# Kernel optimization log

Hardware: AMD Instinct MI355X
Metric: run time of the kernel (lower is better)

The kernel has to match this reference:

```python
import jax, jax.numpy as jnp
import numpy as np
import math

N = 131072        # number of query points
IN_DIM = 3
G = 5             # grid_level = num_sin_layers - 2
F = 8             # feature_dims per level
W = 256           # hidden width (ffenc_dims[1:])
OUT = 64          # num_outputs
BOUND = 1.0
BASE_SIGMA = 1.0
EXP_SIGMA = 2.0
SIN_W0 = 5.0      # multires - 1 = n_levels - 1


def setup_inputs() -> dict:
    key = jax.random.key(0)
    ks = jax.random.split(key, 9)
    in_pos = jax.random.uniform(ks[0], (N, IN_DIM), jnp.float32, -BOUND, BOUND)
    grid_feats = jax.random.normal(ks[1], (N, G * F), jnp.float32) * 0.01  # grid_embed_std
    ffn_A = jax.random.normal(ks[2], (G, F, W), jnp.float32)
    # SIREN-style inits (scaled normals approximating uniform SIREN init ranges)
    W0 = jax.random.normal(ks[3], (IN_DIM, W), jnp.float32) / IN_DIM
    b0 = jax.random.normal(ks[4], (W,), jnp.float32) * 0.01
    Wh = jax.random.normal(ks[5], (G, W, W), jnp.float32) * (math.sqrt(6.0 / W) / SIN_W0)
    bh = jax.random.normal(ks[6], (G, W), jnp.float32) * 0.01
    Wh_high = jax.random.normal(ks[7], (G, W, OUT), jnp.float32) * (math.sqrt(6.0 / W) / SIN_W0)
    bh_high = jax.random.normal(ks[8], (G, OUT), jnp.float32) * 0.01
    return {"in_pos": in_pos, "grid_feats": grid_feats, "ffn_A": ffn_A,
            "W0": W0, "b0": b0, "Wh": Wh, "bh": bh,
            "Wh_high": Wh_high, "bh_high": bh_high}


def reference(in_pos, grid_feats, ffn_A, W0, b0, Wh, bh, Wh_high, bh_high):
    sigmas = BASE_SIGMA * (EXP_SIGMA ** jnp.arange(G, dtype=jnp.float32))  # [G]
    embed = lambda h: jnp.sin(SIN_W0 * h)  # dim-preserving periodic embedding

    x = in_pos / BOUND                                   # [N, 3]
    # grid branch: per-level Fourier projection of hash-grid features
    gx = jnp.transpose(grid_feats.reshape(-1, G, F), (1, 0, 2))  # [G, N, F]
    ffn = ffn_A * sigmas[:, None, None]                   # [G, F, W]
    gx = jnp.sin((2.0 * math.pi) * jnp.einsum('gnf,gfw->gnw', gx, ffn))  # [G, N, W]

    # SIREN branch, layer 0
    x = embed(x @ W0 + b0)                                # [N, W]
    x_out = jnp.zeros((x.shape[0], OUT), dtype=x.dtype)
    for l in range(G):  # layers 1 .. num_sin_layers-2
        x = embed(x @ Wh[l] + bh[l])                      # [N, W]
        x = gx[l] + x                                     # grid residual
        x_out = x_out + embed(x @ Wh_high[l] + bh_high[l])
    return x_out
```

## Files before the change

### kernel.cpp

```cpp
#include <hip/hip_runtime.h>


#define TM 32
#define XSTRIDE 264
#define GSTRIDE 48
#define K5 0.79577471545947667f

typedef __attribute__((ext_vector_type(8))) _Float16 v8h;
typedef __attribute__((ext_vector_type(2))) __fp16 hw2;
typedef __attribute__((ext_vector_type(4))) float v4f;
typedef __attribute__((ext_vector_type(16))) float v16f;

#define MFMA16H(a, b, c) __builtin_amdgcn_mfma_f32_16x16x32_f16(a, b, c, 0, 0, 0)
#define MFMA32H(a, b, c) __builtin_amdgcn_mfma_f32_32x32x16_f16(a, b, c, 0, 0, 0)

__device__ __forceinline__ float sin_rev(float u) {
#if __has_builtin(__builtin_amdgcn_fractf)
    return __builtin_amdgcn_sinf(__builtin_amdgcn_fractf(u));
#else
    return __builtin_amdgcn_sinf(u - floorf(u));
#endif
}

__device__ __forceinline__ short f16s(float x) {
    _Float16 hh = (_Float16)x;
    return __builtin_bit_cast(short, hh);
}

__device__ __forceinline__ unsigned int split_pack_f16(float x) {
    hw2 c = __builtin_amdgcn_cvt_pkrtz(x, x);
    float hf = (float)c[0];
    float d = x - hf;
    hw2 p = __builtin_amdgcn_cvt_pkrtz(x, d);
    return __builtin_bit_cast(unsigned int, p);
}

__device__ __forceinline__ void split_f16_rn(float x, short& h, short& l) {
    _Float16 hh = (_Float16)x;
    float hf = (float)hh;
    _Float16 ll = (_Float16)(x - hf);
    h = __builtin_bit_cast(short, hh);
    l = __builtin_bit_cast(short, ll);
}

__global__ __launch_bounds__(256) void ffb_pack(
    const float* __restrict__ Wh, const float* __restrict__ Whh,
    const float* __restrict__ ffnA,
    short* __restrict__ wh, short* __restrict__ whh,
    short* __restrict__ gf_hi, short* __restrict__ gf_lo)
{
    int t = blockIdx.x * 256 + threadIdx.x;
    if (t < 40960) {
        int lane = t & 63, nt = (t >> 6) & 7, kb = (t >> 9) & 15, l = t >> 13;
        int n = nt * 32 + (lane & 31);
        int k0 = kb * 16 + (lane >> 5) * 8;
        short hs[8];
        #pragma unroll
        for (int jj = 0; jj < 8; jj++)
            hs[jj] = f16s(Wh[(l * 256 + k0 + jj) * 256 + n] * K5);
        *(v8h*)(wh + t * 8) = *(v8h*)hs;
    } else if (t < 51200) {
        int t2 = t - 40960;
        int lane = t2 & 63, nt = (t2 >> 6) & 3, kb = (t2 >> 8) & 7, l = t2 >> 11;
        int n = nt * 16 + (lane & 15);
        int k0 = kb * 32 + (lane >> 4) * 8;
        short hs[8];
        #pragma unroll
        for (int jj = 0; jj < 8; jj++)
            hs[jj] = f16s(Whh[(l * 256 + k0 + jj) * 64 + n] * K5);
        *(v8h*)(whh + t2 * 8) = *(v8h*)hs;
    } else if (t < 53760) {
        int t3 = t - 51200;
        int lane = t3 & 63, nt = (t3 >> 6) & 7, l = t3 >> 9;
        int n = nt * 32 + (lane & 31);
        short hs[8], ls[8];
        #pragma unroll
        for (int jj = 0; jj < 8; jj++)
            split_f16_rn(ffnA[(l * 8 + jj) * 256 + n] * (float)(1 << l),
                         hs[jj], ls[jj]);
        *(v8h*)(gf_hi + t3 * 8) = *(v8h*)hs;
        *(v8h*)(gf_lo + t3 * 8) = *(v8h*)ls;
    }
}

__global__ __launch_bounds__(256, 4) void ffb_main(
    const float* __restrict__ pos, const float* __restrict__ gfeat,
    const float* __restrict__ W0, const float* __restrict__ b0,
    const float* __restrict__ bh, const float* __restrict__ bhh,
    const short* __restrict__ wh, const short* __restrict__ whh,
    const short* __restrict__ gf_hi, const short* __restrict__ gf_lo,
    float* __restrict__ out)
{
    __shared__ __align__(16) short s_x[TM * XSTRIDE];
    __shared__ __align__(16) short s_gh[TM * GSTRIDE];
    __shared__ __align__(16) short s_gl[TM * GSTRIDE];
    __shared__ float s_pos[TM * 3];

    const int tid = threadIdx.x;
    const int row0 = blockIdx.x * TM;
    const int lane = tid & 63;
    const int w = tid >> 6;
    const int i = lane & 15;
    const int q = lane >> 4;
    const int m32 = lane & 31;
    const int h = lane >> 5;

    if (tid < TM * 3) s_pos[tid] = pos[row0 * 3 + tid];
    for (int k2 = tid; k2 < TM * 40; k2 += 256) {
        int r = k2 / 40, f = k2 % 40;
        unsigned int dw = split_pack_f16(gfeat[row0 * 40 + k2]);
        s_gh[r * GSTRIDE + f] = (short)(dw & 0xffffu);
        s_gl[r * GSTRIDE + f] = (short)(dw >> 16);
    }
    __syncthreads();

    {
        const int c = tid;
        const float w00 = W0[c], w01 = W0[256 + c], w02 = W0[512 + c], bc = b0[c];
        #pragma unroll 4
        for (int r = 0; r < TM; r++) {
            float d = s_pos[r * 3 + 0] * w00 + s_pos[r * 3 + 1] * w01
                    + s_pos[r * 3 + 2] * w02 + bc;
            s_x[r * XSTRIDE + c] = f16s(sin_rev(d * K5));
        }
    }
    __syncthreads();

    float cout[2][4];
    #pragma unroll
    for (int m = 0; m < 2; m++)
        #pragma unroll
        for (int r = 0; r < 4; r++) cout[m][r] = 0.f;

    const int a1off = m32 * XSTRIDE + h * 8;
    const int a2off0 = i * XSTRIDE + q * 8;
    const int a2off1 = (16 + i) * XSTRIDE + q * 8;

    for (int l = 0; l < 5; l++) {
        const float bias0 = bh[l * 256 + w * 64 + m32] * K5;
        const float bias1 = bh[l * 256 + w * 64 + 32 + m32] * K5;
        v16f C1[2];
        #pragma unroll
        for (int r = 0; r < 16; r++) { C1[0][r] = bias0; C1[1][r] = bias1; }
        v8h gb0h = *(const v8h*)(gf_hi + ((l * 8 + w * 2 + 0) * 64 + lane) * 8);
        v8h gb1h = *(const v8h*)(gf_hi + ((l * 8 + w * 2 + 1) * 64 + lane) * 8);
        v8h gb0l = *(const v8h*)(gf_lo + ((l * 8 + w * 2 + 0) * 64 + lane) * 8);
        v8h gb1l = *(const v8h*)(gf_lo + ((l * 8 + w * 2 + 1) * 64 + lane) * 8);

        {
            const short* bp = wh + l * 65536 + (2 * w) * 512 + lane * 8;
            v8h bc0 = *(const v8h*)(bp);
            v8h bc1 = *(const v8h*)(bp + 512);
            #pragma unroll
            for (int kb = 0; kb < 16; kb++) {
                const int kn = (kb < 15) ? (kb + 1) : 15;
                v8h bn0 = *(const v8h*)(bp + kn * 4096);
                v8h bn1 = *(const v8h*)(bp + kn * 4096 + 512);
                v8h ah = *(const v8h*)&s_x[a1off + kb * 16];
                C1[0] = MFMA32H(ah, bc0, C1[0]);
                C1[1] = MFMA32H(ah, bc1, C1[1]);
                bc0 = bn0; bc1 = bn1;
            }
        }
        __syncthreads();

        const short* gp = (lane < 32) ? s_gh : s_gl;
        v8h ga = *(const v8h*)&gp[m32 * GSTRIDE + l * 8];
        #pragma unroll
        for (int t = 0; t < 2; t++) {
            v16f Z = {};
            v16f G = MFMA32H(ga, (t ? gb1h : gb0h), Z);
            G = MFMA32H(ga, (t ? gb1l : gb0l), G);
            const int col = w * 64 + t * 32 + m32;
            #pragma unroll
            for (int r = 0; r < 16; r++) {
                const int row = (r & 3) + 8 * (r >> 2) + 4 * h;
                float v = sin_rev(C1[t][r]) + sin_rev(G[r]);
                s_x[row * XSTRIDE + col] = f16s(v);
            }
        }
        __syncthreads();

        const float b2 = bhh[l * 64 + w * 16 + i] * K5;
        v4f C2[2];
        C2[0] = (v4f){b2, b2, b2, b2};
        C2[1] = (v4f){b2, b2, b2, b2};
        {
            const short* bp = whh + l * 16384 + w * 512 + lane * 8;
            v8h bc = *(const v8h*)(bp);
            #pragma unroll
            for (int kb = 0; kb < 8; kb++) {
                const int kn = (kb < 7) ? (kb + 1) : 7;
                v8h bn = *(const v8h*)(bp + kn * 2048);
                v8h a0 = *(const v8h*)&s_x[a2off0 + kb * 32];
                v8h a1 = *(const v8h*)&s_x[a2off1 + kb * 32];
                C2[0] = MFMA16H(a0, bc, C2[0]);
                C2[1] = MFMA16H(a1, bc, C2[1]);
                bc = bn;
            }
        }
        #pragma unroll
        for (int m = 0; m < 2; m++)
            #pragma unroll
            for (int r = 0; r < 4; r++)
                cout[m][r] += sin_rev(C2[m][r]);
    }

    #pragma unroll
    for (int m = 0; m < 2; m++)
        #pragma unroll
        for (int r = 0; r < 4; r++)
            out[(row0 + m * 16 + q * 4 + r) * 64 + w * 16 + i] = cout[m][r];
}

extern "C" void kernel_launch(void* const* d_in, const int* in_sizes, int n_in,
                              void* d_out, int out_size, void* d_ws, size_t ws_size,
                              hipStream_t stream) {
    const float* pos   = (const float*)d_in[0];
    const float* gfeat = (const float*)d_in[1];
    const float* ffnA  = (const float*)d_in[2];
    const float* W0    = (const float*)d_in[3];
    const float* b0    = (const float*)d_in[4];
    const float* Wh    = (const float*)d_in[5];
    const float* bh    = (const float*)d_in[6];
    const float* Whh   = (const float*)d_in[7];
    const float* bhh   = (const float*)d_in[8];
    float* out = (float*)d_out;
    const int N = in_sizes[0] / 3;

    short* wh    = (short*)d_ws;
    short* whh   = wh + 327680;
    short* gf_hi = whh + 81920;
    short* gf_lo = gf_hi + 20480;

    ffb_pack<<<210, 256, 0, stream>>>(Wh, Whh, ffnA, wh, whh, gf_hi, gf_lo);
    ffb_main<<<N / TM, 256, 0, stream>>>(pos, gfeat, W0, b0, bh, bhh,
                                         wh, whh, gf_hi, gf_lo, out);
}
```

Measured before the change: 265.3 us.

## Double row tile to 64 per block to reuse weight fragments across two M tiles

Raises rows per block from 32 to 64, so each wave loads the packed weight fragments once and feeds them to twice as many MFMAs in both the hidden and output GEMMs. This halves global/L2 weight traffic per row. It also deepens the weight prefetch to two k-steps ahead with a 3-slot register ring. In exchange it doubles LDS and accumulator registers and lowers the occupancy target from 4 to 3 blocks per CU, and it halves the grid size.

```diff
diff --git a/kernel.cpp b/kernel.cpp
--- a/kernel.cpp
+++ b/kernel.cpp
@@ -1,7 +1,7 @@
 #include <hip/hip_runtime.h>
 
 
-#define TM 32
+#define TM 64
 #define XSTRIDE 264
 #define GSTRIDE 48
 #define K5 0.79577471545947667f
@@ -83,7 +83,7 @@
     }
 }
 
-__global__ __launch_bounds__(256, 4) void ffb_main(
+__global__ __launch_bounds__(256, 3) void ffb_main(
     const float* __restrict__ pos, const float* __restrict__ gfeat,
     const float* __restrict__ W0, const float* __restrict__ b0,
     const float* __restrict__ bh, const float* __restrict__ bhh,
@@ -126,22 +126,24 @@
     }
     __syncthreads();
 
-    float cout[2][4];
+    float cout[4][4];
     #pragma unroll
-    for (int m = 0; m < 2; m++)
+    for (int m = 0; m < 4; m++)
         #pragma unroll
         for (int r = 0; r < 4; r++) cout[m][r] = 0.f;
 
-    const int a1off = m32 * XSTRIDE + h * 8;
-    const int a2off0 = i * XSTRIDE + q * 8;
-    const int a2off1 = (16 + i) * XSTRIDE + q * 8;
+    const int a1off0 = m32 * XSTRIDE + h * 8;
+    const int a1off1 = (32 + m32) * XSTRIDE + h * 8;
 
     for (int l = 0; l < 5; l++) {
         const float bias0 = bh[l * 256 + w * 64 + m32] * K5;
         const float bias1 = bh[l * 256 + w * 64 + 32 + m32] * K5;
-        v16f C1[2];
-        #pragma unroll
-        for (int r = 0; r < 16; r++) { C1[0][r] = bias0; C1[1][r] = bias1; }
+        v16f C1[2][2];
+        #pragma unroll
+        for (int r = 0; r < 16; r++) {
+            C1[0][0][r] = bias0; C1[1][0][r] = bias0;
+            C1[0][1][r] = bias1; C1[1][1][r] = bias1;
+        }
         v8h gb0h = *(const v8h*)(gf_hi + ((l * 8 + w * 2 + 0) * 64 + lane) * 8);
         v8h gb1h = *(const v8h*)(gf_hi + ((l * 8 + w * 2 + 1) * 64 + lane) * 8);
         v8h gb0l = *(const v8h*)(gf_lo + ((l * 8 + w * 2 + 0) * 64 + lane) * 8);
@@ -149,42 +151,52 @@
 
         {
             const short* bp = wh + l * 65536 + (2 * w) * 512 + lane * 8;
-            v8h bc0 = *(const v8h*)(bp);
-            v8h bc1 = *(const v8h*)(bp + 512);
+            v8h rb0[3], rb1[3];
+            rb0[0] = *(const v8h*)(bp);
+            rb1[0] = *(const v8h*)(bp + 512);
+            rb0[1] = *(const v8h*)(bp + 4096);
+            rb1[1] = *(const v8h*)(bp + 4096 + 512);
             #pragma unroll
             for (int kb = 0; kb < 16; kb++) {
-                const int kn = (kb < 15) ? (kb + 1) : 15;
-                v8h bn0 = *(const v8h*)(bp + kn * 4096);
-                v8h bn1 = *(const v8h*)(bp + kn * 4096 + 512);
-                v8h ah = *(const v8h*)&s_x[a1off + kb * 16];
-                C1[0] = MFMA32H(ah, bc0, C1[0]);
-                C1[1] = MFMA32H(ah, bc1, C1[1]);
-                bc0 = bn0; bc1 = bn1;
+                if (kb + 2 < 16) {
+                    rb0[(kb + 2) % 3] = *(const v8h*)(bp + (kb + 2) * 4096);
+                    rb1[(kb + 2) % 3] = *(const v8h*)(bp + (kb + 2) * 4096 + 512);
+                }
+                v8h a0 = *(const v8h*)&s_x[a1off0 + kb * 16];
+                v8h a1 = *(const v8h*)&s_x[a1off1 + kb * 16];
+                v8h bc0 = rb0[kb % 3], bc1 = rb1[kb % 3];
+                C1[0][0] = MFMA32H(a0, bc0, C1[0][0]);
+                C1[0][1] = MFMA32H(a0, bc1, C1[0][1]);
+                C1[1][0] = MFMA32H(a1, bc0, C1[1][0]);
+                C1[1][1] = MFMA32H(a1, bc1, C1[1][1]);
             }
         }
         __syncthreads();
 
         const short* gp = (lane < 32) ? s_gh : s_gl;
-        v8h ga = *(const v8h*)&gp[m32 * GSTRIDE + l * 8];
-        #pragma unroll
-        for (int t = 0; t < 2; t++) {
-            v16f Z = {};
-            v16f G = MFMA32H(ga, (t ? gb1h : gb0h), Z);
-            G = MFMA32H(ga, (t ? gb1l : gb0l), G);
-            const int col = w * 64 + t * 32 + m32;
-            #pragma unroll
-            for (int r = 0; r < 16; r++) {
-                const int row = (r & 3) + 8 * (r >> 2) + 4 * h;
-                float v = sin_rev(C1[t][r]) + sin_rev(G[r]);
-                s_x[row * XSTRIDE + col] = f16s(v);
+        #pragma unroll
+        for (int m = 0; m < 2; m++) {
+            v8h ga = *(const v8h*)&gp[(m * 32 + m32) * GSTRIDE + l * 8];
+            #pragma unroll
+            for (int t = 0; t < 2; t++) {
+                v16f Z = {};
+                v16f G = MFMA32H(ga, (t ? gb1h : gb0h), Z);
+                G = MFMA32H(ga, (t ? gb1l : gb0l), G);
+                const int col = w * 64 + t * 32 + m32;
+                #pragma unroll
+                for (int r = 0; r < 16; r++) {
+                    const int row = m * 32 + (r & 3) + 8 * (r >> 2) + 4 * h;
+                    float v = sin_rev(C1[m][t][r]) + sin_rev(G[r]);
+                    s_x[row * XSTRIDE + col] = f16s(v);
+                }
             }
         }
         __syncthreads();
 
         const float b2 = bhh[l * 64 + w * 16 + i] * K5;
-        v4f C2[2];
-        C2[0] = (v4f){b2, b2, b2, b2};
-        C2[1] = (v4f){b2, b2, b2, b2};
+        v4f C2[4];
+        #pragma unroll
+        for (int m = 0; m < 4; m++) C2[m] = (v4f){b2, b2, b2, b2};
         {
             const short* bp = whh + l * 16384 + w * 512 + lane * 8;
             v8h bc = *(const v8h*)(bp);
@@ -192,22 +204,23 @@
             for (int kb = 0; kb < 8; kb++) {
                 const int kn = (kb < 7) ? (kb + 1) : 7;
                 v8h bn = *(const v8h*)(bp + kn * 2048);
-                v8h a0 = *(const v8h*)&s_x[a2off0 + kb * 32];
-                v8h a1 = *(const v8h*)&s_x[a2off1 + kb * 32];
-                C2[0] = MFMA16H(a0, bc, C2[0]);
-                C2[1] = MFMA16H(a1, bc, C2[1]);
+                #pragma unroll
+                for (int m = 0; m < 4; m++) {
+                    v8h a = *(const v8h*)&s_x[(m * 16 + i) * XSTRIDE + q * 8 + kb * 32];
+                    C2[m] = MFMA16H(a, bc, C2[m]);
+                }
                 bc = bn;
             }
         }
         #pragma unroll
-        for (int m = 0; m < 2; m++)
+        for (int m = 0; m < 4; m++)
             #pragma unroll
             for (int r = 0; r < 4; r++)
                 cout[m][r] += sin_rev(C2[m][r]);
     }
 
     #pragma unroll
-    for (int m = 0; m < 2; m++)
+    for (int m = 0; m < 4; m++)
         #pragma unroll
         for (int r = 0; r < 4; r++)
             out[(row0 + m * 16 + q * 4 + r) * 64 + w * 16 + i] = cout[m][r];
```

Measured after the change: 249.3 us. 1.06x faster.
